# Kernel optimization log

Hardware: AMD Instinct MI355X
Metric: run time of the kernel (lower is better)

Reference implementation:

```python
import jax, jax.numpy as jnp
import numpy as np


def setup_inputs() -> dict:
    key = jax.random.key(0)
    ks = jax.random.split(key, 8)
    B, Tq, S, H = 32, 4, 2048, 1024
    return {
        "query": jax.random.normal(ks[0], (B, Tq, H), dtype=jnp.float32),
        "keys": jax.random.normal(ks[1], (S, B, 2 * H), dtype=jnp.float32),
        "Wa_w": jax.random.normal(ks[2], (H, H), dtype=jnp.float32) * 0.02,
        "Wa_b": jax.random.normal(ks[3], (H,), dtype=jnp.float32) * 0.02,
        "Ua_w": jax.random.normal(ks[4], (H, 2 * H), dtype=jnp.float32) * 0.02,
        "Ua_b": jax.random.normal(ks[5], (H,), dtype=jnp.float32) * 0.02,
        "Va_w": jax.random.normal(ks[6], (1, H), dtype=jnp.float32) * 0.02,
        "Va_b": jax.random.normal(ks[7], (1,), dtype=jnp.float32) * 0.02,
    }


def reference(query, keys, Wa_w, Wa_b, Ua_w, Ua_b, Va_w, Va_b):
    # query: [B, Tq, H] -> last step [B, 1, H]
    q = query[:, -1:, :]
    # keys: [S, B, 2H] -> [B, S, 2H]
    k = jnp.transpose(keys, (1, 0, 2))
    # Additive attention scores: Va(tanh(Wa(q) + Ua(k)))
    wq = q @ Wa_w.T + Wa_b                      # [B, 1, H]
    uk = k @ Ua_w.T + Ua_b                      # [B, S, H]
    scores = jnp.tanh(wq + uk) @ Va_w.T + Va_b  # [B, S, 1]
    scores = jnp.transpose(scores, (0, 2, 1))   # [B, 1, S]
    weights = jax.nn.softmax(scores, axis=-1)   # [B, 1, S]
    context = jnp.einsum('bqs,bsd->bqd', weights, k)  # [B, 1, 2H]
    return (context, weights)
```

## Files before the change

kernel.cpp:

```cpp
#include <hip/hip_runtime.h>
#include <hip/hip_bf16.h>

typedef __attribute__((ext_vector_type(4))) float f32x4;
typedef __attribute__((ext_vector_type(8))) short short8;

#define B_   32
#define S_   2048
#define H_   1024
#define D2_  2048
#define BM   256
#define BN   256
#define BK   64
#define NKT  32
#define TILE_SH 16384


__device__ __forceinline__ short f2bf(float f) {
  unsigned u = __float_as_uint(f);
  u = (u + 0x7fffu + ((u >> 16) & 1u)) >> 16;
  return (short)u;
}

__device__ __forceinline__ float bf2f(short s) {
  return __uint_as_float(((unsigned)(unsigned short)s) << 16);
}

__device__ __forceinline__ short8 cvt8(f32x4 a, f32x4 b) {
  short8 o;
  o[0] = f2bf(a.x); o[1] = f2bf(a.y); o[2] = f2bf(a.z); o[3] = f2bf(a.w);
  o[4] = f2bf(b.x); o[5] = f2bf(b.y); o[6] = f2bf(b.z); o[7] = f2bf(b.w);
  return o;
}

__device__ __forceinline__ float fast_tanh(float x) {
  float e = __builtin_amdgcn_exp2f(x * 2.885390081777927f);
  return 1.0f - 2.0f * __builtin_amdgcn_rcpf(e + 1.0f);
}

__device__ __forceinline__ void gload16(const short* g, short* l) {
  __builtin_amdgcn_global_load_lds((const __attribute__((address_space(1))) void*)g,
                                   (__attribute__((address_space(3))) void*)l, 16, 0, 0);
}

__global__ void k_convert_ua(const float* __restrict__ src, short* __restrict__ dst) {
  int idx = blockIdx.x * 256 + threadIdx.x;
  int wu  = idx & 2047;
  int kt  = (idx >> 11) & 31;
  int nt  = idx >> 16;
  int kh  = wu >> 10;
  int row = (wu >> 2) & 255;
  int sl  = wu & 3;
  int q   = sl ^ ((row >> 1) & 3);
  const float* s = src + (size_t)(nt * 256 + row) * D2_ + kt * 64 + kh * 32 + q * 8;
  f32x4 a = *(const f32x4*)s;
  f32x4 b = *(const f32x4*)(s + 4);
  *(short8*)(dst + (size_t)idx * 8) = cvt8(a, b);
}

__global__ void k_convert_keys(const float* __restrict__ src, short* __restrict__ dst) {
  int idx = blockIdx.x * 256 + threadIdx.x;
  int wu  = idx & 2047;
  int kt  = (idx >> 11) & 31;
  int mt  = idx >> 16;
  int kh  = wu >> 10;
  int row = (wu >> 2) & 255;
  int sl  = wu & 3;
  int q   = sl ^ ((row >> 1) & 3);
  const float* s = src + (size_t)(mt * 256 + row) * D2_ + kt * 64 + kh * 32 + q * 8;
  f32x4 a = *(const f32x4*)s;
  f32x4 b = *(const f32x4*)(s + 4);
  *(short8*)(dst + (size_t)idx * 8) = cvt8(a, b);
}

__global__ void k_wq(const float* __restrict__ query, const float* __restrict__ Wa_w,
                     const float* __restrict__ Wa_b, const float* __restrict__ Ua_b,
                     float* __restrict__ wqb) {
  int b = blockIdx.x;
  int hc = blockIdx.y;
  int t = threadIdx.x;
  __shared__ float q[H_];
  for (int i = t; i < H_; i += 256) q[i] = query[(size_t)b * (4 * H_) + 3 * H_ + i];
  __syncthreads();
  int h = hc * 128 + (t >> 1);
  int kh = (t & 1) * 512;
  const float* wr = Wa_w + (size_t)h * H_ + kh;
  float acc = 0.f;
  #pragma unroll 8
  for (int k = 0; k < 512; k += 4) {
    f32x4 wv = *(const f32x4*)(wr + k);
    acc += wv.x * q[kh + k] + wv.y * q[kh + k + 1] + wv.z * q[kh + k + 2] + wv.w * q[kh + k + 3];
  }
  acc += __shfl_xor(acc, 1);
  if ((t & 1) == 0) wqb[b * H_ + h] = acc + Wa_b[h] + Ua_b[h];
}

#define MFMA_C(mb)                                                                                 \
  __builtin_amdgcn_s_setprio(1);                                                                   \
  _Pragma("unroll")                                                                                \
  for (int n = 0; n < 4; ++n) {                                                                    \
    _Pragma("unroll")                                                                              \
    for (int i = 0; i < 4; ++i)                                                                    \
      acc[(mb) + i][n] =                                                                           \
          __builtin_amdgcn_mfma_f32_16x16x32_bf16(af[i], bf[n], acc[(mb) + i][n], 0, 0, 0);        \
  }                                                                                                \
  __builtin_amdgcn_s_setprio(0);

__global__ __launch_bounds__(512, 2) void k_gemm_score(
    const short* __restrict__ keys_bf, const short* __restrict__ uab_t,
    const float* __restrict__ wqb, const float* __restrict__ va,
    float* __restrict__ scores_p) {
  __shared__ short As[2][TILE_SH];
  __shared__ short Bs[2][TILE_SH];

  const int bid = blockIdx.x;
  const int g = (bid & 7) * 128 + (bid >> 3);
  const int mt = g >> 2;
  const int nt = g & 3;
  const int r0 = mt * BM;
  const int h0 = nt * BN;

  const int t = threadIdx.x;
  const int lane = t & 63;
  const int w = t >> 6;
  const int wm = w >> 2;
  const int wn = w & 3;

  f32x4 acc[8][4] = {};

  const short* abase = keys_bf + (size_t)mt * (NKT * TILE_SH) + t * 8;
  const short* bbase = uab_t  + (size_t)nt * (NKT * TILE_SH) + t * 8;
  const int wu = w * 512;

  const int lr = lane & 15;
  const int lq = lane >> 4;
  const int slot = lq ^ ((lr >> 1) & 3);
  const int ar_ = (wm * 128 + lr) * 32 + slot * 8;
  const int br_ = (wn * 64 + lr) * 32 + slot * 8;

  {
    #pragma unroll
    for (int j = 0; j < 4; ++j) gload16(abase + j * 4096, &As[0][j * 4096 + wu]);
    #pragma unroll
    for (int j = 0; j < 4; ++j) gload16(bbase + j * 4096, &Bs[0][j * 4096 + wu]);
    asm volatile("s_waitcnt vmcnt(0)" ::: "memory");
    __builtin_amdgcn_s_barrier();
  }

  short8 af[4], bf[4];

  #pragma unroll 1
  for (int kt = 0; kt < NKT; ++kt) {
    const int cb = kt & 1;
    const bool stage = (kt < NKT - 1);
    const short* Ac = As[cb];
    const short* Bc = Bs[cb];
    const short* anext = abase + (size_t)(kt + 1) * TILE_SH;
    const short* bnext = bbase + (size_t)(kt + 1) * TILE_SH;
    short* Anb = &As[cb ^ 1][0];
    short* Bnb = &Bs[cb ^ 1][0];

    #pragma unroll
    for (int n = 0; n < 4; ++n) bf[n] = *(const short8*)&Bc[br_ + n * 512];
    #pragma unroll
    for (int i = 0; i < 4; ++i) af[i] = *(const short8*)&Ac[ar_ + i * 512];
    if (stage) {
      gload16(anext + 0 * 4096, Anb + 0 * 4096 + wu);
      gload16(anext + 1 * 4096, Anb + 1 * 4096 + wu);
    }
    __builtin_amdgcn_s_barrier();
    asm volatile("s_waitcnt lgkmcnt(0)" ::: "memory");
    MFMA_C(0)
    __builtin_amdgcn_s_barrier();

    #pragma unroll
    for (int i = 0; i < 4; ++i) af[i] = *(const short8*)&Ac[ar_ + (4 + i) * 512];
    if (stage) {
      gload16(bnext + 0 * 4096, Bnb + 0 * 4096 + wu);
      gload16(bnext + 1 * 4096, Bnb + 1 * 4096 + wu);
    }
    __builtin_amdgcn_s_barrier();
    asm volatile("s_waitcnt lgkmcnt(0)" ::: "memory");
    MFMA_C(4)
    if (stage) { asm volatile("s_waitcnt vmcnt(4)" ::: "memory"); }
    else       { asm volatile("s_waitcnt vmcnt(0)" ::: "memory"); }
    __builtin_amdgcn_s_barrier();

    #pragma unroll
    for (int n = 0; n < 4; ++n) bf[n] = *(const short8*)&Bc[br_ + 8192 + n * 512];
    #pragma unroll
    for (int i = 0; i < 4; ++i) af[i] = *(const short8*)&Ac[ar_ + 8192 + i * 512];
    if (stage) {
      gload16(anext + 2 * 4096, Anb + 2 * 4096 + wu);
      gload16(anext + 3 * 4096, Anb + 3 * 4096 + wu);
    }
    __builtin_amdgcn_s_barrier();
    asm volatile("s_waitcnt lgkmcnt(0)" ::: "memory");
    MFMA_C(0)
    __builtin_amdgcn_s_barrier();

    #pragma unroll
    for (int i = 0; i < 4; ++i) af[i] = *(const short8*)&Ac[ar_ + 8192 + (4 + i) * 512];
    if (stage) {
      gload16(bnext + 2 * 4096, Bnb + 2 * 4096 + wu);
      gload16(bnext + 3 * 4096, Bnb + 3 * 4096 + wu);
    }
    __builtin_amdgcn_s_barrier();
    asm volatile("s_waitcnt lgkmcnt(0)" ::: "memory");
    MFMA_C(4)
    if (stage) { asm volatile("s_waitcnt vmcnt(4)" ::: "memory"); }
    __builtin_amdgcn_s_barrier();
  }

  const int lgrp = lane >> 4;
  const int lc = lane & 15;
  float vah[4];
  #pragma unroll
  for (int n = 0; n < 4; ++n) vah[n] = va[h0 + wn * 64 + n * 16 + lc];
  #pragma unroll
  for (int m = 0; m < 8; ++m) {
    #pragma unroll
    for (int reg = 0; reg < 4; ++reg) {
      int row = wm * 128 + m * 16 + lgrp * 4 + reg;
      int r = r0 + row;
      int bb = r & (B_ - 1);
      const float* wrow = wqb + bb * H_ + h0 + wn * 64 + lc;
      float s = 0.f;
      #pragma unroll
      for (int n = 0; n < 4; ++n)
        s += vah[n] * fast_tanh(acc[m][n][reg] + wrow[n * 16]);
      s += __shfl_xor(s, 1);
      s += __shfl_xor(s, 2);
      s += __shfl_xor(s, 4);
      s += __shfl_xor(s, 8);
      if (lc == 0) scores_p[(size_t)r * 16 + nt * 4 + wn] = s;
    }
  }
}

__global__ __launch_bounds__(512, 2) void k_gemm_rs(
    const float* __restrict__ keys, const short* __restrict__ uab_t,
    const float* __restrict__ wqb, const float* __restrict__ va,
    float* __restrict__ scores_p) {
  __shared__ short As[2][TILE_SH];
  __shared__ short Bs[2][TILE_SH];
  const int bid = blockIdx.x;
  const int g = (bid & 7) * 128 + (bid >> 3);
  const int mt = g >> 2;
  const int nt = g & 3;
  const int r0 = mt * BM;
  const int h0 = nt * BN;
  const int t = threadIdx.x;
  const int lane = t & 63;
  const int w = t >> 6;
  const int wm = w >> 2;
  const int wn = w & 3;
  f32x4 acc[8][4] = {};
  const int arow = t >> 1;
  const int ahalf = t & 1;
  const float* abase = keys + (size_t)(r0 + arow) * D2_ + ahalf * 32;
  int awoff[4];
  #pragma unroll
  for (int j = 0; j < 4; ++j)
    awoff[j] = (ahalf * 1024 + arow * 4 + (j ^ ((arow >> 1) & 3))) * 8;
  const short* bbase = uab_t + (size_t)nt * NKT * TILE_SH + t * 8;
  const int wu = w * 512;
  const int lr = lane & 15;
  const int lq = lane >> 4;
  const int slot = lq ^ ((lr >> 1) & 3);
  const int ar_ = (wm * 128 + lr) * 32 + slot * 8;
  const int br_ = (wn * 64 + lr) * 32 + slot * 8;
  {
    f32x4 v[8];
    #pragma unroll
    for (int j = 0; j < 8; ++j) v[j] = *(const f32x4*)(abase + j * 4);
    #pragma unroll
    for (int j = 0; j < 4; ++j)
      *(short8*)&As[0][awoff[j]] = cvt8(v[2 * j], v[2 * j + 1]);
    #pragma unroll
    for (int j = 0; j < 4; ++j) gload16(bbase + j * 4096, &Bs[0][j * 4096 + wu]);
    asm volatile("s_waitcnt vmcnt(0) lgkmcnt(0)" ::: "memory");
    __builtin_amdgcn_s_barrier();
  }
  f32x4 av[8];
  short8 af[4], bf[4];
  #pragma unroll 1
  for (int kt = 0; kt < NKT; ++kt) {
    const int cb = kt & 1;
    const bool stage = (kt < NKT - 1);
    const float* anext = abase + (kt + 1) * BK;
    const short* bnext = bbase + (size_t)(kt + 1) * TILE_SH;
    short* Bnb = &Bs[cb ^ 1][0];
    const short* Ac = As[cb];
    const short* Bc = Bs[cb];

    #pragma unroll
    for (int n = 0; n < 4; ++n) bf[n] = *(const short8*)&Bc[br_ + n * 512];
    #pragma unroll
    for (int i = 0; i < 4; ++i) af[i] = *(const short8*)&Ac[ar_ + i * 512];
    if (stage) {
      #pragma unroll
      for (int j = 0; j < 8; ++j) av[j] = *(const f32x4*)(anext + j * 4);
    }
    __builtin_amdgcn_s_barrier();
    asm volatile("s_waitcnt lgkmcnt(0)" ::: "memory");
    MFMA_C(0)
    __builtin_amdgcn_s_barrier();

    #pragma unroll
    for (int i = 0; i < 4; ++i) af[i] = *(const short8*)&Ac[ar_ + (4 + i) * 512];
    if (stage) {
      gload16(bnext + 0 * 4096, Bnb + 0 * 4096 + wu);
      gload16(bnext + 1 * 4096, Bnb + 1 * 4096 + wu);
    }
    __builtin_amdgcn_s_barrier();
    asm volatile("s_waitcnt lgkmcnt(0)" ::: "memory");
    MFMA_C(4)
    __builtin_amdgcn_s_barrier();

    #pragma unroll
    for (int n = 0; n < 4; ++n) bf[n] = *(const short8*)&Bc[br_ + 8192 + n * 512];
    #pragma unroll
    for (int i = 0; i < 4; ++i) af[i] = *(const short8*)&Ac[ar_ + 8192 + i * 512];
    if (stage) {
      gload16(bnext + 2 * 4096, Bnb + 2 * 4096 + wu);
      gload16(bnext + 3 * 4096, Bnb + 3 * 4096 + wu);
    }
    __builtin_amdgcn_s_barrier();
    asm volatile("s_waitcnt lgkmcnt(0)" ::: "memory");
    MFMA_C(0)
    __builtin_amdgcn_s_barrier();

    #pragma unroll
    for (int i = 0; i < 4; ++i) af[i] = *(const short8*)&Ac[ar_ + 8192 + (4 + i) * 512];
    if (stage) {
      #pragma unroll
      for (int j = 0; j < 4; ++j)
        *(short8*)&As[cb ^ 1][awoff[j]] = cvt8(av[2 * j], av[2 * j + 1]);
    }
    __builtin_amdgcn_s_barrier();
    asm volatile("s_waitcnt lgkmcnt(0)" ::: "memory");
    MFMA_C(4)
    asm volatile("s_waitcnt vmcnt(0) lgkmcnt(0)" ::: "memory");
    __builtin_amdgcn_s_barrier();
  }
  const int lgrp = lane >> 4;
  const int lc = lane & 15;
  float vah[4];
  #pragma unroll
  for (int n = 0; n < 4; ++n) vah[n] = va[h0 + wn * 64 + n * 16 + lc];
  #pragma unroll
  for (int m = 0; m < 8; ++m) {
    #pragma unroll
    for (int reg = 0; reg < 4; ++reg) {
      int row = wm * 128 + m * 16 + lgrp * 4 + reg;
      int r = r0 + row;
      int bb = r & (B_ - 1);
      const float* wrow = wqb + bb * H_ + h0 + wn * 64 + lc;
      float s = 0.f;
      #pragma unroll
      for (int n = 0; n < 4; ++n)
        s += vah[n] * fast_tanh(acc[m][n][reg] + wrow[n * 16]);
      s += __shfl_xor(s, 1);
      s += __shfl_xor(s, 2);
      s += __shfl_xor(s, 4);
      s += __shfl_xor(s, 8);
      if (lc == 0) scores_p[(size_t)r * 16 + nt * 4 + wn] = s;
    }
  }
}

__global__ void k_softmax(const float* __restrict__ scores_p, float* __restrict__ out) {
  int b = blockIdx.x;
  int t = threadIdx.x;
  __shared__ float sc[S_];
  __shared__ float red[4];
  float lmax = -3.4e38f;
  #pragma unroll
  for (int i = 0; i < 8; ++i) {
    int s = t + i * 256;
    const float* p = scores_p + ((size_t)s * B_ + b) * 16;
    f32x4 p0 = *(const f32x4*)p;
    f32x4 p1 = *(const f32x4*)(p + 4);
    f32x4 p2 = *(const f32x4*)(p + 8);
    f32x4 p3 = *(const f32x4*)(p + 12);
    f32x4 ps = p0 + p1 + p2 + p3;
    float v = ps.x + ps.y + ps.z + ps.w;
    sc[s] = v;
    lmax = fmaxf(lmax, v);
  }
  #pragma unroll
  for (int o = 32; o >= 1; o >>= 1) lmax = fmaxf(lmax, __shfl_xor(lmax, o));
  if ((t & 63) == 0) red[t >> 6] = lmax;
  __syncthreads();
  float gmax = fmaxf(fmaxf(red[0], red[1]), fmaxf(red[2], red[3]));
  __syncthreads();
  float lsum = 0.f;
  #pragma unroll
  for (int i = 0; i < 8; ++i) {
    int s = t + i * 256;
    float e = __builtin_amdgcn_exp2f((sc[s] - gmax) * 1.4426950408889634f);
    sc[s] = e;
    lsum += e;
  }
  #pragma unroll
  for (int o = 32; o >= 1; o >>= 1) lsum += __shfl_xor(lsum, o);
  if ((t & 63) == 0) red[t >> 6] = lsum;
  __syncthreads();
  float inv = 1.0f / (red[0] + red[1] + red[2] + red[3]);
  for (int i = 0; i < 8; ++i) {
    int s = t + i * 256;
    out[(size_t)65536 + b * S_ + s] = sc[s] * inv;
  }
}

__global__ __launch_bounds__(256) void k_ctx_partial_bf(const short* __restrict__ keys_bf,
                                                        const float* __restrict__ wts,
                                                        float* __restrict__ cp) {
  int b = blockIdx.x;
  int scn2 = blockIdx.y;
  int t = threadIdx.x;
  __shared__ float wl[128];
  int s0 = scn2 * 128;
  if (t < 128) wl[t] = wts[b * S_ + s0 + t];
  __syncthreads();
  const int k = t * 8;
  const int kt = k >> 6;
  const int kh = (k >> 5) & 1;
  const int q  = (k >> 3) & 3;
  const int slot = q ^ ((b >> 1) & 3);
  int roff[8];
  #pragma unroll
  for (int j = 0; j < 8; ++j) roff[j] = (j * 32 + b) * 32 + slot * 8;
  f32x4 accA = {}, accB = {};
  for (int c = 0; c < 16; ++c) {
    const short* tb = keys_bf + ((size_t)((scn2 * 16 + c) * 32 + kt) * 2048 + (size_t)kh * 1024) * 8;
    #pragma unroll
    for (int j = 0; j < 8; ++j) {
      short8 v = *(const short8*)(tb + roff[j]);
      float wgt = wl[c * 8 + j];
      accA.x += wgt * bf2f(v[0]); accA.y += wgt * bf2f(v[1]);
      accA.z += wgt * bf2f(v[2]); accA.w += wgt * bf2f(v[3]);
      accB.x += wgt * bf2f(v[4]); accB.y += wgt * bf2f(v[5]);
      accB.z += wgt * bf2f(v[6]); accB.w += wgt * bf2f(v[7]);
    }
  }
  float* o = cp + ((size_t)scn2 * B_ + b) * D2_ + k;
  *(f32x4*)o = accA;
  *(f32x4*)(o + 4) = accB;
}

__global__ void k_ctx_partial(const float* __restrict__ keys, const float* __restrict__ wts,
                              float* __restrict__ cp) {
  int b = blockIdx.x;
  int dc = blockIdx.y;
  int scn = blockIdx.z;
  int t = threadIdx.x;
  __shared__ float wl[256];
  int s0 = scn * 256;
  wl[t] = wts[b * S_ + s0 + t];
  __syncthreads();
  int d = dc * 1024 + t * 4;
  f32x4 acc = {};
  #pragma unroll 4
  for (int i = 0; i < 256; ++i) {
    int s = s0 + i;
    f32x4 kv = *(const f32x4*)(keys + ((size_t)s * B_ + b) * D2_ + d);
    acc += kv * wl[i];
  }
  *(f32x4*)(cp + ((size_t)scn * B_ + b) * D2_ + d) = acc;
}

__global__ void k_ctx_reduce(const float* __restrict__ cp, float* __restrict__ out, int np) {
  int i = blockIdx.x * 256 + threadIdx.x;
  float s = 0.f;
  for (int j = 0; j < np; ++j) s += cp[(size_t)j * 65536 + i];
  out[i] = s;
}

extern "C" void kernel_launch(void* const* d_in, const int* in_sizes, int n_in,
                              void* d_out, int out_size, void* d_ws, size_t ws_size,
                              hipStream_t stream) {
  const float* query = (const float*)d_in[0];
  const float* keys  = (const float*)d_in[1];
  const float* Wa_w  = (const float*)d_in[2];
  const float* Wa_b  = (const float*)d_in[3];
  const float* Ua_w  = (const float*)d_in[4];
  const float* Ua_b  = (const float*)d_in[5];
  const float* Va_w  = (const float*)d_in[6];
  float* out = (float*)d_out;
  char* ws = (char*)d_ws;

  const size_t KEYS_BF_BYTES = 268435456ull;
  const size_t TAIL = 16ull * 1024 * 1024;
  bool big = ws_size >= KEYS_BF_BYTES + TAIL;

  if (big) {
    short* keys_bf = (short*)ws;
    char* base = ws + KEYS_BF_BYTES;
    short* uab_t = (short*)(base);
    float* wqb = (float*)(base + 4u * 1024 * 1024);
    float* sp  = (float*)(base + 4u * 1024 * 1024 + 128 * 1024);
    float* cp  = (float*)(base + 8u * 1024 * 1024 + 256 * 1024);

    hipLaunchKernelGGL(k_convert_ua, dim3(1024), dim3(256), 0, stream, Ua_w, uab_t);
    hipLaunchKernelGGL(k_convert_keys, dim3(65536), dim3(256), 0, stream, keys, keys_bf);
    hipLaunchKernelGGL(k_wq, dim3(32, 8), dim3(256), 0, stream, query, Wa_w, Wa_b, Ua_b, wqb);
    hipLaunchKernelGGL(k_gemm_score, dim3(1024), dim3(512), 0, stream, keys_bf, uab_t, wqb, Va_w, sp);
    hipLaunchKernelGGL(k_softmax, dim3(32), dim3(256), 0, stream, sp, out);
    hipLaunchKernelGGL(k_ctx_partial_bf, dim3(32, 16), dim3(256), 0, stream, keys_bf, out + 65536, cp);
    hipLaunchKernelGGL(k_ctx_reduce, dim3(256), dim3(256), 0, stream, cp, out, 16);
  } else {
    short* uab_t = (short*)(ws);
    float* wqb = (float*)(ws + 4u * 1024 * 1024);
    float* sp  = (float*)(ws + 4u * 1024 * 1024 + 128 * 1024);
    float* cp  = (float*)(ws + 8u * 1024 * 1024 + 256 * 1024);

    hipLaunchKernelGGL(k_convert_ua, dim3(1024), dim3(256), 0, stream, Ua_w, uab_t);
    hipLaunchKernelGGL(k_wq, dim3(32, 8), dim3(256), 0, stream, query, Wa_w, Wa_b, Ua_b, wqb);
    hipLaunchKernelGGL(k_gemm_rs, dim3(1024), dim3(512), 0, stream, keys, uab_t, wqb, Va_w, sp);
    hipLaunchKernelGGL(k_softmax, dim3(32), dim3(256), 0, stream, sp, out);
    hipLaunchKernelGGL(k_ctx_partial, dim3(32, 2, 8), dim3(256), 0, stream, keys, out + 65536, cp);
    hipLaunchKernelGGL(k_ctx_reduce, dim3(256), dim3(256), 0, stream, cp, out, 8);
  }
}
```

Before: 551.0 us.

## Double-buffer LDS fragment registers in score GEMM and use fp32 context path

The main GEMM loop now ping-pongs between two sets of A/B register fragments, so LDS reads for the next sub-step are issued before the current MFMA block and waited on with partial lgkmcnt counts. Loads of the next tile's first fragments move into the previous iteration, and the final k-tile is peeled. The aim is to hide LDS latency behind MFMA work and to drop full lgkmcnt(0) stalls. Separately, the bf16 context kernel is removed and the big-workspace path now reads fp32 keys with 8 partials. That doubles context read bytes but gives exact fp32 context; the reduce loop is fixed at 8 and unrolled.

```diff
diff --git a/kernel.cpp b/kernel.cpp
--- a/kernel.cpp
+++ b/kernel.cpp
@@ -19,10 +19,6 @@
   unsigned u = __float_as_uint(f);
   u = (u + 0x7fffu + ((u >> 16) & 1u)) >> 16;
   return (short)u;
-}
-
-__device__ __forceinline__ float bf2f(short s) {
-  return __uint_as_float(((unsigned)(unsigned short)s) << 16);
 }
 
 __device__ __forceinline__ short8 cvt8(f32x4 a, f32x4 b) {
@@ -94,16 +90,24 @@
   if ((t & 1) == 0) wqb[b * H_ + h] = acc + Wa_b[h] + Ua_b[h];
 }
 
-#define MFMA_C(mb)                                                                                 \
-  __builtin_amdgcn_s_setprio(1);                                                                   \
-  _Pragma("unroll")                                                                                \
-  for (int n = 0; n < 4; ++n) {                                                                    \
-    _Pragma("unroll")                                                                              \
-    for (int i = 0; i < 4; ++i)                                                                    \
-      acc[(mb) + i][n] =                                                                           \
-          __builtin_amdgcn_mfma_f32_16x16x32_bf16(af[i], bf[n], acc[(mb) + i][n], 0, 0, 0);        \
-  }                                                                                                \
+#define MCL(mb, AF, BF)                                                                           \
+  __builtin_amdgcn_s_setprio(1);                                                                  \
+  _Pragma("unroll")                                                                               \
+  for (int n = 0; n < 4; ++n) {                                                                   \
+    _Pragma("unroll")                                                                             \
+    for (int i = 0; i < 4; ++i)                                                                   \
+      acc[(mb) + i][n] =                                                                          \
+          __builtin_amdgcn_mfma_f32_16x16x32_bf16(AF[i], BF[n], acc[(mb) + i][n], 0, 0, 0);       \
+  }                                                                                               \
   __builtin_amdgcn_s_setprio(0);
+
+#define LGKM4  asm volatile("s_waitcnt lgkmcnt(4)" ::: "memory"); __builtin_amdgcn_sched_barrier(0);
+#define LGKM8  asm volatile("s_waitcnt lgkmcnt(8)" ::: "memory"); __builtin_amdgcn_sched_barrier(0);
+#define LGKM0  asm volatile("s_waitcnt lgkmcnt(0)" ::: "memory"); __builtin_amdgcn_sched_barrier(0);
+#define VM2    asm volatile("s_waitcnt vmcnt(2)" ::: "memory");
+#define VM0    asm volatile("s_waitcnt vmcnt(0)" ::: "memory");
+#define BAR    __builtin_amdgcn_s_barrier();
+#define SBAR0  __builtin_amdgcn_sched_barrier(0);
 
 __global__ __launch_bounds__(512, 2) void k_gemm_score(
     const short* __restrict__ keys_bf, const short* __restrict__ uab_t,
@@ -137,78 +141,106 @@
   const int ar_ = (wm * 128 + lr) * 32 + slot * 8;
   const int br_ = (wn * 64 + lr) * 32 + slot * 8;
 
+  short8 afX[4], afY[4], bfX[4], bfY[4];
+
   {
     #pragma unroll
     for (int j = 0; j < 4; ++j) gload16(abase + j * 4096, &As[0][j * 4096 + wu]);
     #pragma unroll
     for (int j = 0; j < 4; ++j) gload16(bbase + j * 4096, &Bs[0][j * 4096 + wu]);
-    asm volatile("s_waitcnt vmcnt(0)" ::: "memory");
-    __builtin_amdgcn_s_barrier();
-  }
-
-  short8 af[4], bf[4];
+    VM0
+    BAR
+    SBAR0
+    #pragma unroll
+    for (int n = 0; n < 4; ++n) bfX[n] = *(const short8*)&Bs[0][br_ + n * 512];
+    #pragma unroll
+    for (int i = 0; i < 4; ++i) afX[i] = *(const short8*)&As[0][ar_ + i * 512];
+  }
 
   #pragma unroll 1
-  for (int kt = 0; kt < NKT; ++kt) {
+  for (int kt = 0; kt < NKT - 1; ++kt) {
     const int cb = kt & 1;
-    const bool stage = (kt < NKT - 1);
     const short* Ac = As[cb];
     const short* Bc = Bs[cb];
+    const short* Anb = &As[cb ^ 1][0];
+    const short* Bnb = &Bs[cb ^ 1][0];
+    short* Anbw = &As[cb ^ 1][0];
+    short* Bnbw = &Bs[cb ^ 1][0];
     const short* anext = abase + (size_t)(kt + 1) * TILE_SH;
     const short* bnext = bbase + (size_t)(kt + 1) * TILE_SH;
-    short* Anb = &As[cb ^ 1][0];
-    short* Bnb = &Bs[cb ^ 1][0];
-
-    #pragma unroll
-    for (int n = 0; n < 4; ++n) bf[n] = *(const short8*)&Bc[br_ + n * 512];
-    #pragma unroll
-    for (int i = 0; i < 4; ++i) af[i] = *(const short8*)&Ac[ar_ + i * 512];
-    if (stage) {
-      gload16(anext + 0 * 4096, Anb + 0 * 4096 + wu);
-      gload16(anext + 1 * 4096, Anb + 1 * 4096 + wu);
-    }
-    __builtin_amdgcn_s_barrier();
-    asm volatile("s_waitcnt lgkmcnt(0)" ::: "memory");
-    MFMA_C(0)
-    __builtin_amdgcn_s_barrier();
-
-    #pragma unroll
-    for (int i = 0; i < 4; ++i) af[i] = *(const short8*)&Ac[ar_ + (4 + i) * 512];
-    if (stage) {
-      gload16(bnext + 0 * 4096, Bnb + 0 * 4096 + wu);
-      gload16(bnext + 1 * 4096, Bnb + 1 * 4096 + wu);
-    }
-    __builtin_amdgcn_s_barrier();
-    asm volatile("s_waitcnt lgkmcnt(0)" ::: "memory");
-    MFMA_C(4)
-    if (stage) { asm volatile("s_waitcnt vmcnt(4)" ::: "memory"); }
-    else       { asm volatile("s_waitcnt vmcnt(0)" ::: "memory"); }
-    __builtin_amdgcn_s_barrier();
-
-    #pragma unroll
-    for (int n = 0; n < 4; ++n) bf[n] = *(const short8*)&Bc[br_ + 8192 + n * 512];
-    #pragma unroll
-    for (int i = 0; i < 4; ++i) af[i] = *(const short8*)&Ac[ar_ + 8192 + i * 512];
-    if (stage) {
-      gload16(anext + 2 * 4096, Anb + 2 * 4096 + wu);
-      gload16(anext + 3 * 4096, Anb + 3 * 4096 + wu);
-    }
-    __builtin_amdgcn_s_barrier();
-    asm volatile("s_waitcnt lgkmcnt(0)" ::: "memory");
-    MFMA_C(0)
-    __builtin_amdgcn_s_barrier();
-
-    #pragma unroll
-    for (int i = 0; i < 4; ++i) af[i] = *(const short8*)&Ac[ar_ + 8192 + (4 + i) * 512];
-    if (stage) {
-      gload16(bnext + 2 * 4096, Bnb + 2 * 4096 + wu);
-      gload16(bnext + 3 * 4096, Bnb + 3 * 4096 + wu);
-    }
-    __builtin_amdgcn_s_barrier();
-    asm volatile("s_waitcnt lgkmcnt(0)" ::: "memory");
-    MFMA_C(4)
-    if (stage) { asm volatile("s_waitcnt vmcnt(4)" ::: "memory"); }
-    __builtin_amdgcn_s_barrier();
+
+    #pragma unroll
+    for (int i = 0; i < 4; ++i) afY[i] = *(const short8*)&Ac[ar_ + (4 + i) * 512];
+    gload16(anext + 0 * 4096, Anbw + 0 * 4096 + wu);
+    gload16(anext + 1 * 4096, Anbw + 1 * 4096 + wu);
+    BAR
+    LGKM4
+    MCL(0, afX, bfX)
+    VM2
+    BAR
+    SBAR0
+
+    #pragma unroll
+    for (int n = 0; n < 4; ++n) bfY[n] = *(const short8*)&Bc[br_ + 8192 + n * 512];
+    #pragma unroll
+    for (int i = 0; i < 4; ++i) afX[i] = *(const short8*)&Ac[ar_ + 8192 + i * 512];
+    gload16(bnext + 0 * 4096, Bnbw + 0 * 4096 + wu);
+    gload16(bnext + 1 * 4096, Bnbw + 1 * 4096 + wu);
+    BAR
+    LGKM8
+    MCL(4, afY, bfX)
+    BAR
+
+    #pragma unroll
+    for (int i = 0; i < 4; ++i) afY[i] = *(const short8*)&Ac[ar_ + 8192 + (4 + i) * 512];
+    gload16(anext + 2 * 4096, Anbw + 2 * 4096 + wu);
+    gload16(anext + 3 * 4096, Anbw + 3 * 4096 + wu);
+    BAR
+    LGKM4
+    MCL(0, afX, bfY)
+    VM2
+    BAR
+    SBAR0
+
+    #pragma unroll
+    for (int n = 0; n < 4; ++n) bfX[n] = *(const short8*)&Bnb[br_ + n * 512];
+    #pragma unroll
+    for (int i = 0; i < 4; ++i) afX[i] = *(const short8*)&Anb[ar_ + i * 512];
+    gload16(bnext + 2 * 4096, Bnbw + 2 * 4096 + wu);
+    gload16(bnext + 3 * 4096, Bnbw + 3 * 4096 + wu);
+    BAR
+    LGKM8
+    MCL(4, afY, bfY)
+    BAR
+  }
+
+  {
+    const short* Ac = As[1];
+    const short* Bc = Bs[1];
+    #pragma unroll
+    for (int i = 0; i < 4; ++i) afY[i] = *(const short8*)&Ac[ar_ + (4 + i) * 512];
+    BAR
+    LGKM4
+    MCL(0, afX, bfX)
+    VM0
+    BAR
+    SBAR0
+    #pragma unroll
+    for (int n = 0; n < 4; ++n) bfY[n] = *(const short8*)&Bc[br_ + 8192 + n * 512];
+    #pragma unroll
+    for (int i = 0; i < 4; ++i) afX[i] = *(const short8*)&Ac[ar_ + 8192 + i * 512];
+    BAR
+    LGKM8
+    MCL(4, afY, bfX)
+    BAR
+    #pragma unroll
+    for (int i = 0; i < 4; ++i) afY[i] = *(const short8*)&Ac[ar_ + 8192 + (4 + i) * 512];
+    BAR
+    LGKM4
+    MCL(0, afX, bfY)
+    BAR
+    LGKM0
+    MCL(4, afY, bfY)
   }
 
   const int lgrp = lane >> 4;
@@ -269,6 +301,7 @@
   const int slot = lq ^ ((lr >> 1) & 3);
   const int ar_ = (wm * 128 + lr) * 32 + slot * 8;
   const int br_ = (wn * 64 + lr) * 32 + slot * 8;
+  short8 af[4], bf[4];
   {
     f32x4 v[8];
     #pragma unroll
@@ -282,7 +315,6 @@
     __builtin_amdgcn_s_barrier();
   }
   f32x4 av[8];
-  short8 af[4], bf[4];
   #pragma unroll 1
   for (int kt = 0; kt < NKT; ++kt) {
     const int cb = kt & 1;
@@ -302,8 +334,8 @@
       for (int j = 0; j < 8; ++j) av[j] = *(const f32x4*)(anext + j * 4);
     }
     __builtin_amdgcn_s_barrier();
-    asm volatile("s_waitcnt lgkmcnt(0)" ::: "memory");
-    MFMA_C(0)
+    LGKM0
+    MCL(0, af, bf)
     __builtin_amdgcn_s_barrier();
 
     #pragma unroll
@@ -313,8 +345,8 @@
       gload16(bnext + 1 * 4096, Bnb + 1 * 4096 + wu);
     }
     __builtin_amdgcn_s_barrier();
-    asm volatile("s_waitcnt lgkmcnt(0)" ::: "memory");
-    MFMA_C(4)
+    LGKM0
+    MCL(4, af, bf)
     __builtin_amdgcn_s_barrier();
 
     #pragma unroll
@@ -326,8 +358,8 @@
       gload16(bnext + 3 * 4096, Bnb + 3 * 4096 + wu);
     }
     __builtin_amdgcn_s_barrier();
-    asm volatile("s_waitcnt lgkmcnt(0)" ::: "memory");
-    MFMA_C(0)
+    LGKM0
+    MCL(0, af, bf)
     __builtin_amdgcn_s_barrier();
 
     #pragma unroll
@@ -338,8 +370,8 @@
         *(short8*)&As[cb ^ 1][awoff[j]] = cvt8(av[2 * j], av[2 * j + 1]);
     }
     __builtin_amdgcn_s_barrier();
-    asm volatile("s_waitcnt lgkmcnt(0)" ::: "memory");
-    MFMA_C(4)
+    LGKM0
+    MCL(4, af, bf)
     asm volatile("s_waitcnt vmcnt(0) lgkmcnt(0)" ::: "memory");
     __builtin_amdgcn_s_barrier();
   }
@@ -411,42 +443,6 @@
     int s = t + i * 256;
     out[(size_t)65536 + b * S_ + s] = sc[s] * inv;
   }
-}
-
-__global__ __launch_bounds__(256) void k_ctx_partial_bf(const short* __restrict__ keys_bf,
-                                                        const float* __restrict__ wts,
-                                                        float* __restrict__ cp) {
-  int b = blockIdx.x;
-  int scn2 = blockIdx.y;
-  int t = threadIdx.x;
-  __shared__ float wl[128];
-  int s0 = scn2 * 128;
-  if (t < 128) wl[t] = wts[b * S_ + s0 + t];
-  __syncthreads();
-  const int k = t * 8;
-  const int kt = k >> 6;
-  const int kh = (k >> 5) & 1;
-  const int q  = (k >> 3) & 3;
-  const int slot = q ^ ((b >> 1) & 3);
-  int roff[8];
-  #pragma unroll
-  for (int j = 0; j < 8; ++j) roff[j] = (j * 32 + b) * 32 + slot * 8;
-  f32x4 accA = {}, accB = {};
-  for (int c = 0; c < 16; ++c) {
-    const short* tb = keys_bf + ((size_t)((scn2 * 16 + c) * 32 + kt) * 2048 + (size_t)kh * 1024) * 8;
-    #pragma unroll
-    for (int j = 0; j < 8; ++j) {
-      short8 v = *(const short8*)(tb + roff[j]);
-      float wgt = wl[c * 8 + j];
-      accA.x += wgt * bf2f(v[0]); accA.y += wgt * bf2f(v[1]);
-      accA.z += wgt * bf2f(v[2]); accA.w += wgt * bf2f(v[3]);
-      accB.x += wgt * bf2f(v[4]); accB.y += wgt * bf2f(v[5]);
-      accB.z += wgt * bf2f(v[6]); accB.w += wgt * bf2f(v[7]);
-    }
-  }
-  float* o = cp + ((size_t)scn2 * B_ + b) * D2_ + k;
-  *(f32x4*)o = accA;
-  *(f32x4*)(o + 4) = accB;
 }
 
 __global__ void k_ctx_partial(const float* __restrict__ keys, const float* __restrict__ wts,
@@ -470,10 +466,11 @@
   *(f32x4*)(cp + ((size_t)scn * B_ + b) * D2_ + d) = acc;
 }
 
-__global__ void k_ctx_reduce(const float* __restrict__ cp, float* __restrict__ out, int np) {
+__global__ void k_ctx_reduce(const float* __restrict__ cp, float* __restrict__ out) {
   int i = blockIdx.x * 256 + threadIdx.x;
   float s = 0.f;
-  for (int j = 0; j < np; ++j) s += cp[(size_t)j * 65536 + i];
+  #pragma unroll
+  for (int j = 0; j < 8; ++j) s += cp[(size_t)j * 65536 + i];
   out[i] = s;
 }
 
@@ -507,8 +504,8 @@
     hipLaunchKernelGGL(k_wq, dim3(32, 8), dim3(256), 0, stream, query, Wa_w, Wa_b, Ua_b, wqb);
     hipLaunchKernelGGL(k_gemm_score, dim3(1024), dim3(512), 0, stream, keys_bf, uab_t, wqb, Va_w, sp);
     hipLaunchKernelGGL(k_softmax, dim3(32), dim3(256), 0, stream, sp, out);
-    hipLaunchKernelGGL(k_ctx_partial_bf, dim3(32, 16), dim3(256), 0, stream, keys_bf, out + 65536, cp);
-    hipLaunchKernelGGL(k_ctx_reduce, dim3(256), dim3(256), 0, stream, cp, out, 16);
+    hipLaunchKernelGGL(k_ctx_partial, dim3(32, 2, 8), dim3(256), 0, stream, keys, out + 65536, cp);
+    hipLaunchKernelGGL(k_ctx_reduce, dim3(256), dim3(256), 0, stream, cp, out);
   } else {
     short* uab_t = (short*)(ws);
     float* wqb = (float*)(ws + 4u * 1024 * 1024);
@@ -520,6 +517,6 @@
     hipLaunchKernelGGL(k_gemm_rs, dim3(1024), dim3(512), 0, stream, keys, uab_t, wqb, Va_w, sp);
     hipLaunchKernelGGL(k_softmax, dim3(32), dim3(256), 0, stream, sp, out);
     hipLaunchKernelGGL(k_ctx_partial, dim3(32, 2, 8), dim3(256), 0, stream, keys, out + 65536, cp);
-    hipLaunchKernelGGL(k_ctx_reduce, dim3(256), dim3(256), 0, stream, cp, out, 8);
-  }
-}
+    hipLaunchKernelGGL(k_ctx_reduce, dim3(256), dim3(256), 0, stream, cp, out);
+  }
+}
```

Result: no change. 555.2 us (+0.8%).
